# Performance work log

Measured on AMD Instinct MI355X. Metric: run time of the kernel, lower is better.

Reference implementation:

```python
import jax, jax.numpy as jnp
import numpy as np

EPS_BN = 1e-5
EPS_NORM = 1e-12


def setup_inputs() -> dict:
    dim, mid, k = 128, 32, 3
    b, h, w = 8, 128, 128
    key = jax.random.key(0)
    ks = jax.random.split(key, 16)
    s = 0.05
    return {
        "x": jax.random.normal(ks[0], (b, dim, h, w), jnp.float32),
        "w_spatial_in": jax.random.normal(ks[1], (dim, dim), jnp.float32) * s,
        "w_dw_spatial": jax.random.normal(ks[2], (dim, 1, k), jnp.float32) * s,
        "w_spatial_out": jax.random.normal(ks[3], (dim, dim), jnp.float32) * s,
        "w_ch_in": jax.random.normal(ks[4], (dim, dim), jnp.float32) * s,
        "w_ch_dw": jax.random.normal(ks[5], (dim, 1, k), jnp.float32) * s,
        "w_ch_out": jax.random.normal(ks[6], (dim, dim), jnp.float32) * s,
        "w_mlp1": jax.random.normal(ks[7], (mid, dim), jnp.float32) * s,
        "b_mlp1": jax.random.normal(ks[8], (mid,), jnp.float32) * s,
        "w_mlp2": jax.random.normal(ks[9], (dim, mid), jnp.float32) * s,
        "b_mlp2": jax.random.normal(ks[10], (dim,), jnp.float32) * s,
        "diff_weight": jnp.float32(1.0),
        "bn_gamma": jnp.ones((dim,), jnp.float32),
        "bn_beta": jnp.zeros((dim,), jnp.float32),
        "w_out_proj": jax.random.normal(ks[11], (dim, dim), jnp.float32) * s,
    }


def _dwconv1d(seq, wk):
    # seq: [b, c, L], wk: [c, 1, k] depthwise, 'same' padding
    c = seq.shape[1]
    k = wk.shape[-1]
    return jax.lax.conv_general_dilated(
        seq, wk, window_strides=(1,), padding=[(k // 2, k // 2)],
        dimension_numbers=("NCH", "OIH", "NCH"), feature_group_count=c)


def _ocs_forward(x, w_spatial_in, w_dw_spatial, w_spatial_out,
                 w_ch_in, w_ch_dw, w_ch_out,
                 w_mlp1, b_mlp1, w_mlp2, b_mlp2,
                 diff_weight, bn_gamma, bn_beta, w_out_proj):
    b, c, h, w = x.shape
    L = h * w
    alpha = beta = eta = 1.0

    # ---- scan indices (4 orders) ----
    idx_row = jnp.arange(L)
    gy, gx = jnp.meshgrid(jnp.arange(h), jnp.arange(w), indexing="ij")
    idx_col = (gx * h + gy).reshape(-1)
    orders = [idx_row, idx_row[::-1], idx_col, idx_col[::-1]]

    x_seq0 = x.reshape(b, c, L).transpose(0, 2, 1)  # [b, L, c]

    def scan(idx):
        s = x_seq0[:, idx]                                   # gather   [b,L,c]
        s = jnp.einsum("blc,oc->blo", s, w_spatial_in)       # linear
        s = _dwconv1d(s.transpose(0, 2, 1), w_dw_spatial)    # dw conv  [b,c,L]
        s = jnp.einsum("bcl,oc->blo", s, w_spatial_out)      # linear   [b,L,c]
        s = s.at[:, idx].set(s[:, jnp.arange(L)]) if False else s[:, jnp.argsort(idx)]  # scatter back (inverse perm)
        return s.transpose(0, 2, 1).reshape(b, c, h, w)

    y_sp = (scan(orders[0]) + scan(orders[1]) + scan(orders[2]) + scan(orders[3])) * 0.25

    # ---- channel branch ----
    seq = x.reshape(b, c, L)
    seq = jnp.einsum("oc,bcl->bol", w_ch_in, seq)
    seq = _dwconv1d(seq, w_ch_dw)
    seq = jnp.einsum("oc,bcl->bol", w_ch_out, seq)
    gap = x.mean((2, 3))                                     # [b,c]
    gap = gap / jnp.maximum(jnp.linalg.norm(gap, axis=1, keepdims=True), EPS_NORM)
    m = jnp.einsum("bi,bj->bij", gap, gap)                   # [b,c,c]
    seq_agg = jnp.einsum("bij,bjl->bil", m, seq)             # [b,c,L]
    h1 = jax.nn.silu(jnp.einsum("mc,bcl->bml", w_mlp1, seq_agg) + b_mlp1[None, :, None])
    y_ch = (jnp.einsum("cm,bml->bcl", w_mlp2, h1) + b_mlp2[None, :, None]).reshape(b, c, h, w)

    # ---- difference branch (reflect-pad 4-neighbor abs diff) ----
    p = jnp.pad(x, ((0, 0), (0, 0), (1, 1), (1, 1)), mode="reflect")
    cx = p[:, :, 1:-1, 1:-1]
    diff = (jnp.abs(cx - p[:, :, 1:-1, :-2]) + jnp.abs(cx - p[:, :, 1:-1, 2:])
            + jnp.abs(cx - p[:, :, :-2, 1:-1]) + jnp.abs(cx - p[:, :, 2:, 1:-1])) * 0.25
    y_diff = x + diff_weight * diff

    # ---- combine, 1x1 proj, batchnorm (training-mode batch stats) ----
    y = alpha * y_sp + beta * y_ch + eta * y_diff
    y = jnp.einsum("oc,bchw->bohw", w_out_proj, y)
    mu = y.mean((0, 2, 3))
    var = y.var((0, 2, 3))
    y = (y - mu[None, :, None, None]) * jax.lax.rsqrt(var + EPS_BN)[None, :, None, None]
    y = y * bn_gamma[None, :, None, None] + bn_beta[None, :, None, None]
    return y


def reference(x, w_spatial_in, w_dw_spatial, w_spatial_out, w_ch_in, w_ch_dw,
              w_ch_out, w_mlp1, b_mlp1, w_mlp2, b_mlp2, diff_weight,
              bn_gamma, bn_beta, w_out_proj):
    return _ocs_forward(x, w_spatial_in, w_dw_spatial, w_spatial_out,
                        w_ch_in, w_ch_dw, w_ch_out, w_mlp1, b_mlp1,
                        w_mlp2, b_mlp2, diff_weight, bn_gamma, bn_beta,
                        w_out_proj)
```

## Files before the change

kernel.cpp:

```cpp
#include <hip/hip_runtime.h>
#include <hip/hip_bf16.h>

#define C 128
#define L 16384
#define B 8
#define MID 32
#define NBL (B * L)

typedef unsigned short ushort_t;
typedef __attribute__((ext_vector_type(8))) short s8v;
typedef __attribute__((ext_vector_type(4))) float f4v;
typedef __attribute__((ext_vector_type(8))) float f8v;

__device__ __forceinline__ unsigned short f2bf(float f) {
    union { float f; unsigned int u; } a; a.f = f;
    unsigned int u = a.u;
    return (unsigned short)((u + 0x7fffu + ((u >> 16) & 1u)) >> 16);
}

__device__ __forceinline__ f8v unp8(s8v v) {
    f8v f;
#pragma unroll
    for (int j = 0; j < 8; j++) f[j] = __uint_as_float(((unsigned int)(unsigned short)v[j]) << 16);
    return f;
}

__device__ __forceinline__ f8v ldf8(const float* p) {
    float4 a = *(const float4*)p;
    float4 b = *(const float4*)(p + 4);
    f8v f;
    f[0] = a.x; f[1] = a.y; f[2] = a.z; f[3] = a.w;
    f[4] = b.x; f[5] = b.y; f[6] = b.z; f[7] = b.w;
    return f;
}

__device__ __forceinline__ int widx(int slot, int o, int w) {
    return ((slot * 8 + (o >> 4)) * 64 + (w >> 3) * 16 + (o & 15)) * 8 + (w & 7);
}

__global__ __launch_bounds__(256) void k_cvt(const float* __restrict__ x,
                                             ushort_t* __restrict__ xb,
                                             float* __restrict__ gap) {
    __shared__ float xs[64][129];
    const int bid = blockIdx.x;
    const int b = bid >> 8;
    const int l0 = (bid & 255) * 64;
    const int tid = threadIdx.x;
    const int rr = tid >> 4;
    const int col = (tid & 15) * 4;
#pragma unroll
    for (int pass = 0; pass < 8; pass++) {
        const int c = pass * 16 + rr;
        float4 v = *(const float4*)(x + ((size_t)(b * C + c)) * L + l0 + col);
        xs[col + 0][c] = v.x; xs[col + 1][c] = v.y;
        xs[col + 2][c] = v.z; xs[col + 3][c] = v.w;
    }
    __syncthreads();
    {
        const int c = tid >> 1, h = tid & 1;
        float s = 0.f;
#pragma unroll
        for (int k = 0; k < 32; k++) s += xs[h * 32 + k][c];
        s += __shfl_xor(s, 1);
        if (h == 0) atomicAdd(&gap[b * C + c], s);
    }
    const int l = tid & 63, quarter = tid >> 6, cb = quarter * 32;
    union { ushort_t hh[32]; uint4 qv[4]; } u;
#pragma unroll
    for (int k = 0; k < 32; k++) u.hh[k] = f2bf(xs[l][cb + k]);
    uint4* dst = (uint4*)(xb + ((size_t)(b * L + l0 + l)) * C + cb);
#pragma unroll
    for (int k = 0; k < 4; k++) dst[k] = u.qv[k];
}

__global__ __launch_bounds__(128) void k_prep(const float* __restrict__ Win,
                                              const float* __restrict__ Wproj,
                                              const float* __restrict__ Wout,
                                              const float* __restrict__ w2,
                                              const float* __restrict__ b2,
                                              const float* __restrict__ wds,
                                              const float* __restrict__ gap,
                                              const float* __restrict__ w1,
                                              const float* __restrict__ Wco,
                                              const float* __restrict__ wcd,
                                              const float* __restrict__ Wci,
                                              ushort_t* __restrict__ Wf,
                                              float* __restrict__ bp,
                                              float* __restrict__ a,
                                              float* __restrict__ pv) {
    const int bid = blockIdx.x;
    const int c = threadIdx.x;
    if (bid < 128) {
        const int o = bid;
        __shared__ float pr[C];
        __shared__ float wct[C];
        pr[c] = Wproj[o * C + c];
        __syncthreads();
        {
            float s = 0.f;
            for (int k = 0; k < C; k++) s = fmaf(pr[k], Wout[k * C + c], s);
            wct[c] = s;
        }
        __syncthreads();
        float a1 = 0.f, as = 0.f;
        for (int cc = 0; cc < C; cc++) {
            float w = wct[cc];
            float win = Win[cc * C + c];
            a1 = fmaf(w * wds[3 * cc + 1], win, a1);
            as = fmaf(w * (0.25f * (wds[3 * cc] + wds[3 * cc + 2])), win, as);
        }
        const int slot = c >> 5, wi = c & 31;
        Wf[widx(slot, o, wi)] = f2bf(a1);
        Wf[widx(4 + slot, o, wi)] = f2bf(as);
        Wf[widx(8 + slot, o, wi)] = f2bf(pr[c]);
        if (c < MID) {
            float s2 = 0.f;
            for (int k = 0; k < C; k++) s2 = fmaf(pr[k], w2[k * MID + c], s2);
            Wf[widx(12, o, c)] = f2bf(s2);
        }
        if (c == 0) {
            float s3 = 0.f;
            for (int k = 0; k < C; k++) s3 = fmaf(pr[k], b2[k], s3);
            bp[o] = s3;
        }
    } else {
        const int b = bid - 128;
        __shared__ float gl[C];
        __shared__ float red[C];
        __shared__ float gws[C];
        float v = gap[b * C + c] * (1.f / (float)L);
        red[c] = v * v;
        __syncthreads();
        for (int w = 64; w > 0; w >>= 1) {
            if (c < w) red[c] += red[c + w];
            __syncthreads();
        }
        float nrm = fmaxf(sqrtf(red[0]), 1e-12f);
        gl[c] = v / nrm;
        __syncthreads();
        if (c < MID) {
            float s = 0.f;
            for (int k = 0; k < C; k++) s = fmaf(w1[c * C + k], gl[k], s);
            a[b * MID + c] = s;
        }
        {
            float s = 0.f;
            for (int k = 0; k < C; k++) s = fmaf(gl[k], Wco[k * C + c], s);
            gws[c] = s;
        }
        __syncthreads();
        float p0 = 0.f, p1 = 0.f, p2 = 0.f;
        for (int cc = 0; cc < C; cc++) {
            float wv = Wci[cc * C + c];
            float g = gws[cc];
            p0 = fmaf(g * wcd[3 * cc], wv, p0);
            p1 = fmaf(g * wcd[3 * cc + 1], wv, p1);
            p2 = fmaf(g * wcd[3 * cc + 2], wv, p2);
        }
        pv[b * 384 + c] = p0;
        pv[b * 384 + 128 + c] = p1;
        pv[b * 384 + 256 + c] = p2;
    }
}

__global__ __launch_bounds__(1024) __attribute__((amdgpu_waves_per_eu(4, 4)))
void k_fused(const ushort_t* __restrict__ xb,
             const ushort_t* __restrict__ Wf,
             const float* __restrict__ pv,
             const float* __restrict__ a,
             const float* __restrict__ b1,
             const float* __restrict__ pdw,
             const float* __restrict__ bp,
             float* __restrict__ outp,
             float* __restrict__ stats) {
    __shared__ ushort_t wlf[53248];
    __shared__ float sdst[C];
    __shared__ float sdsq[C];
    const int tid = threadIdx.x;
    int bid = blockIdx.x;
    bid = (bid & 7) * 128 + (bid >> 3);
    const int b = bid >> 7;
    const int y = bid & 127;

#pragma unroll
    for (int i = 0; i < 7; i++) {
        int idx = tid + i * 1024;
        if (idx < 6656) ((uint4*)wlf)[idx] = ((const uint4*)Wf)[idx];
    }
    if (tid < C) { sdst[tid] = 0.f; sdsq[tid] = 0.f; }

    const int wave = tid >> 6, lane = tid & 63;
    const int half = wave & 1;
    const int lg = wave >> 1;
    const int n = lane & 15, q = lane >> 4;
    const int xg = lg * 16 + n;
    const int l = y * 128 + xg;
    const size_t rb = (size_t)b * L;

    const int rL = (l > 0) ? (l - 1) : -1;
    const int rR = (l < L - 1) ? (l + 1) : -1;
    const int rU = (y > 0) ? (l - 128) : ((xg > 0) ? (16256 + xg - 1) : -1);
    const int rD = (y < 127) ? (l + 128) : ((xg < 127) ? (xg + 1) : -1);
    const ushort_t* xrow = xb + (rb + l) * C;
    const ushort_t* prL = xb + (rb + ((rL >= 0) ? rL : 0)) * C;
    const ushort_t* prR = xb + (rb + ((rR >= 0) ? rR : 0)) * C;
    const ushort_t* prU = xb + (rb + ((rU >= 0) ? rU : 0)) * C;
    const ushort_t* prD = xb + (rb + ((rD >= 0) ? rD : 0)) * C;

    const float dwt4 = pdw[0] * 0.25f;

    float s1 = 0.f;
#pragma unroll
    for (int ks = 0; ks < 4; ks++) {
        const int c0 = ks * 32 + q * 8;
        {
            f8v xv = unp8(*(const s8v*)(xrow + c0));
            f8v p = ldf8(pv + b * 384 + 128 + c0);
#pragma unroll
            for (int j = 0; j < 8; j++) s1 = fmaf(p[j], xv[j], s1);
        }
        {
            f8v xv = unp8(*(const s8v*)(prL + c0));
            if (rL < 0) {
#pragma unroll
                for (int j = 0; j < 8; j++) xv[j] = 0.f;
            }
            f8v p = ldf8(pv + b * 384 + c0);
#pragma unroll
            for (int j = 0; j < 8; j++) s1 = fmaf(p[j], xv[j], s1);
        }
        {
            f8v xv = unp8(*(const s8v*)(prR + c0));
            if (rR < 0) {
#pragma unroll
                for (int j = 0; j < 8; j++) xv[j] = 0.f;
            }
            f8v p = ldf8(pv + b * 384 + 256 + c0);
#pragma unroll
            for (int j = 0; j < 8; j++) s1 = fmaf(p[j], xv[j], s1);
        }
    }
    s1 += __shfl_xor(s1, 16);
    s1 += __shfl_xor(s1, 32);

    s8v fs;
    {
        f8v av = ldf8(a + b * MID + q * 8);
        f8v bv = ldf8(b1 + q * 8);
#pragma unroll
        for (int j = 0; j < 8; j++) {
            float pre = fmaf(av[j], s1, bv[j]);
            fs[j] = (short)f2bf(pre / (1.f + __expf(-pre)));
        }
    }

    f4v acc[4];
#pragma unroll
    for (int i = 0; i < 4; i++) acc[i] = (f4v){0.f, 0.f, 0.f, 0.f};

    __syncthreads();

#define AF(slot, mtg) (*(const s8v*)(wlf + ((((slot) * 8 + (mtg)) * 64 + lane) * 8)))

#pragma unroll
    for (int mt = 0; mt < 4; mt++)
        acc[mt] = __builtin_amdgcn_mfma_f32_16x16x32_bf16(AF(12, half * 4 + mt), fs, acc[mt], 0, 0, 0);

#pragma unroll
    for (int t = 0; t < 4; t++) {
        const int r = (t == 0) ? rL : (t == 1) ? rR : (t == 2) ? rU : rD;
        const ushort_t* prow = (t == 0) ? prL : (t == 1) ? prR : (t == 2) ? prU : prD;
#pragma unroll
        for (int ks = 0; ks < 4; ks++) {
            s8v v = *(const s8v*)(prow + ks * 32 + q * 8);
            if (r < 0) v = (s8v){0, 0, 0, 0, 0, 0, 0, 0};
#pragma unroll
            for (int mt = 0; mt < 4; mt++)
                acc[mt] = __builtin_amdgcn_mfma_f32_16x16x32_bf16(AF(4 + ks, half * 4 + mt), v, acc[mt], 0, 0, 0);
        }
    }

#pragma unroll
    for (int ks = 0; ks < 4; ks++) {
        const int c0 = ks * 32 + q * 8;
        s8v vc = *(const s8v*)(xrow + c0);
#pragma unroll
        for (int mt = 0; mt < 4; mt++)
            acc[mt] = __builtin_amdgcn_mfma_f32_16x16x32_bf16(AF(ks, half * 4 + mt), vc, acc[mt], 0, 0, 0);
        f8v xc = unp8(vc);
        f8v d8;
        {
            f8v t1 = unp8(*(const s8v*)(((xg > 0) ? prL : prR) + c0));
#pragma unroll
            for (int j = 0; j < 8; j++) d8[j] = fabsf(xc[j] - t1[j]);
        }
        {
            f8v t1 = unp8(*(const s8v*)(((xg < 127) ? prR : prL) + c0));
#pragma unroll
            for (int j = 0; j < 8; j++) d8[j] += fabsf(xc[j] - t1[j]);
        }
        {
            f8v t1 = unp8(*(const s8v*)(((y > 0) ? prU : prD) + c0));
#pragma unroll
            for (int j = 0; j < 8; j++) d8[j] += fabsf(xc[j] - t1[j]);
        }
        {
            f8v t1 = unp8(*(const s8v*)(((y < 127) ? prD : prU) + c0));
#pragma unroll
            for (int j = 0; j < 8; j++) d8[j] += fabsf(xc[j] - t1[j]);
        }
        s8v vy;
#pragma unroll
        for (int j = 0; j < 8; j++) vy[j] = (short)f2bf(fmaf(dwt4, d8[j], xc[j]));
#pragma unroll
        for (int mt = 0; mt < 4; mt++)
            acc[mt] = __builtin_amdgcn_mfma_f32_16x16x32_bf16(AF(8 + ks, half * 4 + mt), vy, acc[mt], 0, 0, 0);
    }

#undef AF

#pragma unroll
    for (int mt = 0; mt < 4; mt++) {
        const int o0 = (half * 4 + mt) * 16 + q * 4;
        float4 bv4 = *(const float4*)(bp + o0);
#pragma unroll
        for (int i = 0; i < 4; i++) {
            float bai = (i == 0) ? bv4.x : (i == 1) ? bv4.y : (i == 2) ? bv4.z : bv4.w;
            float v = acc[mt][i] + bai;
            outp[((size_t)(b * C + o0 + i)) * L + l] = v;
            float s = v, sq = v * v;
            s += __shfl_xor(s, 1); sq += __shfl_xor(sq, 1);
            s += __shfl_xor(s, 2); sq += __shfl_xor(sq, 2);
            s += __shfl_xor(s, 4); sq += __shfl_xor(sq, 4);
            s += __shfl_xor(s, 8); sq += __shfl_xor(sq, 8);
            if (n == 0) {
                atomicAdd(&sdst[o0 + i], s);
                atomicAdd(&sdsq[o0 + i], sq);
            }
        }
    }
    __syncthreads();
    if (tid < C) {
        atomicAdd(&stats[tid], sdst[tid]);
        atomicAdd(&stats[C + tid], sdsq[tid]);
    }
}

__global__ __launch_bounds__(256) void k_bnapply(float* __restrict__ outp,
                                                 const float* __restrict__ stats,
                                                 const float* __restrict__ gamma,
                                                 const float* __restrict__ beta) {
    int bo = blockIdx.x;
    int o = bo & (C - 1);
    float nn = (float)NBL;
    float mu = stats[o] / nn;
    float var = stats[C + o] / nn - mu * mu;
    float sc = gamma[o] * rsqrtf(var + 1e-5f);
    float sh = fmaf(-mu, sc, beta[o]);
    float4* p = (float4*)(outp + (size_t)bo * L);
    for (int i = threadIdx.x; i < L / 4; i += 256) {
        float4 v = p[i];
        v.x = fmaf(v.x, sc, sh);
        v.y = fmaf(v.y, sc, sh);
        v.z = fmaf(v.z, sc, sh);
        v.w = fmaf(v.w, sc, sh);
        p[i] = v;
    }
}

extern "C" void kernel_launch(void* const* d_in, const int* in_sizes, int n_in,
                              void* d_out, int out_size, void* d_ws, size_t ws_size,
                              hipStream_t stream) {
    const float* x = (const float*)d_in[0];
    const float* Win = (const float*)d_in[1];
    const float* wds = (const float*)d_in[2];
    const float* Wout = (const float*)d_in[3];
    const float* Wci = (const float*)d_in[4];
    const float* wcd = (const float*)d_in[5];
    const float* Wco = (const float*)d_in[6];
    const float* w1 = (const float*)d_in[7];
    const float* b1 = (const float*)d_in[8];
    const float* w2 = (const float*)d_in[9];
    const float* b2 = (const float*)d_in[10];
    const float* pdw = (const float*)d_in[11];
    const float* gamma = (const float*)d_in[12];
    const float* beta = (const float*)d_in[13];
    const float* Wproj = (const float*)d_in[14];

    char* wsb = (char*)d_ws;
    ushort_t* xb = (ushort_t*)wsb;
    ushort_t* Wf = (ushort_t*)(wsb + 33554432);
    char* S = wsb + 176160768;
    float* gap  = (float*)(S + 0);
    float* stats= (float*)(S + 4096);
    float* a    = (float*)(S + 6144);
    float* bp   = (float*)(S + 8192);
    float* pv   = (float*)(S + 12288);
    float* outp = (float*)d_out;

    hipMemsetAsync(S, 0, 5120, stream);
    k_cvt<<<2048, 256, 0, stream>>>(x, xb, gap);
    k_prep<<<136, 128, 0, stream>>>(Win, Wproj, Wout, w2, b2, wds,
                                    gap, w1, Wco, wcd, Wci, Wf, bp, a, pv);
    k_fused<<<1024, 1024, 0, stream>>>(xb, Wf, pv, a, b1, pdw, bp, outp, stats);
    k_bnapply<<<1024, 256, 0, stream>>>(outp, stats, gamma, beta);
}
```

Measured before the change: 329.2 us.

## Split fused kernel by output half and move BN stats to separate pass

```diff
diff --git a/kernel.cpp b/kernel.cpp
--- a/kernel.cpp
+++ b/kernel.cpp
@@ -163,7 +163,7 @@
     }
 }
 
-__global__ __launch_bounds__(1024) __attribute__((amdgpu_waves_per_eu(4, 4)))
+__global__ __launch_bounds__(512) __attribute__((amdgpu_waves_per_eu(6, 6)))
 void k_fused(const ushort_t* __restrict__ xb,
              const ushort_t* __restrict__ Wf,
              const float* __restrict__ pv,
@@ -171,29 +171,27 @@
              const float* __restrict__ b1,
              const float* __restrict__ pdw,
              const float* __restrict__ bp,
-             float* __restrict__ outp,
-             float* __restrict__ stats) {
-    __shared__ ushort_t wlf[53248];
-    __shared__ float sdst[C];
-    __shared__ float sdsq[C];
+             float* __restrict__ outp) {
+    __shared__ ushort_t wlf[26624];
     const int tid = threadIdx.x;
     int bid = blockIdx.x;
-    bid = (bid & 7) * 128 + (bid >> 3);
-    const int b = bid >> 7;
-    const int y = bid & 127;
+    bid = (bid & 7) * 256 + (bid >> 3);
+    const int b = bid >> 8;
+    const int y = (bid >> 1) & 127;
+    const int half = bid & 1;
 
 #pragma unroll
     for (int i = 0; i < 7; i++) {
-        int idx = tid + i * 1024;
-        if (idx < 6656) ((uint4*)wlf)[idx] = ((const uint4*)Wf)[idx];
-    }
-    if (tid < C) { sdst[tid] = 0.f; sdsq[tid] = 0.f; }
+        int idx = tid + i * 512;
+        if (idx < 3328) {
+            int s = idx >> 8, w = idx & 255;
+            ((uint4*)wlf)[s * 256 + w] = ((const uint4*)Wf)[(s * 8 + half * 4) * 64 + w];
+        }
+    }
 
     const int wave = tid >> 6, lane = tid & 63;
-    const int half = wave & 1;
-    const int lg = wave >> 1;
     const int n = lane & 15, q = lane >> 4;
-    const int xg = lg * 16 + n;
+    const int xg = wave * 16 + n;
     const int l = y * 128 + xg;
     const size_t rb = (size_t)b * L;
 
@@ -260,11 +258,11 @@
 
     __syncthreads();
 
-#define AF(slot, mtg) (*(const s8v*)(wlf + ((((slot) * 8 + (mtg)) * 64 + lane) * 8)))
+#define AF(slot, mt) (*(const s8v*)(wlf + ((((slot) * 4 + (mt)) * 64 + lane) * 8)))
 
 #pragma unroll
     for (int mt = 0; mt < 4; mt++)
-        acc[mt] = __builtin_amdgcn_mfma_f32_16x16x32_bf16(AF(12, half * 4 + mt), fs, acc[mt], 0, 0, 0);
+        acc[mt] = __builtin_amdgcn_mfma_f32_16x16x32_bf16(AF(12, mt), fs, acc[mt], 0, 0, 0);
 
 #pragma unroll
     for (int t = 0; t < 4; t++) {
@@ -276,7 +274,7 @@
             if (r < 0) v = (s8v){0, 0, 0, 0, 0, 0, 0, 0};
 #pragma unroll
             for (int mt = 0; mt < 4; mt++)
-                acc[mt] = __builtin_amdgcn_mfma_f32_16x16x32_bf16(AF(4 + ks, half * 4 + mt), v, acc[mt], 0, 0, 0);
+                acc[mt] = __builtin_amdgcn_mfma_f32_16x16x32_bf16(AF(4 + ks, mt), v, acc[mt], 0, 0, 0);
         }
     }
 
@@ -286,7 +284,7 @@
         s8v vc = *(const s8v*)(xrow + c0);
 #pragma unroll
         for (int mt = 0; mt < 4; mt++)
-            acc[mt] = __builtin_amdgcn_mfma_f32_16x16x32_bf16(AF(ks, half * 4 + mt), vc, acc[mt], 0, 0, 0);
+            acc[mt] = __builtin_amdgcn_mfma_f32_16x16x32_bf16(AF(ks, mt), vc, acc[mt], 0, 0, 0);
         f8v xc = unp8(vc);
         f8v d8;
         {
@@ -314,7 +312,7 @@
         for (int j = 0; j < 8; j++) vy[j] = (short)f2bf(fmaf(dwt4, d8[j], xc[j]));
 #pragma unroll
         for (int mt = 0; mt < 4; mt++)
-            acc[mt] = __builtin_amdgcn_mfma_f32_16x16x32_bf16(AF(8 + ks, half * 4 + mt), vy, acc[mt], 0, 0, 0);
+            acc[mt] = __builtin_amdgcn_mfma_f32_16x16x32_bf16(AF(8 + ks, mt), vy, acc[mt], 0, 0, 0);
     }
 
 #undef AF
@@ -326,23 +324,35 @@
 #pragma unroll
         for (int i = 0; i < 4; i++) {
             float bai = (i == 0) ? bv4.x : (i == 1) ? bv4.y : (i == 2) ? bv4.z : bv4.w;
-            float v = acc[mt][i] + bai;
-            outp[((size_t)(b * C + o0 + i)) * L + l] = v;
-            float s = v, sq = v * v;
-            s += __shfl_xor(s, 1); sq += __shfl_xor(sq, 1);
-            s += __shfl_xor(s, 2); sq += __shfl_xor(sq, 2);
-            s += __shfl_xor(s, 4); sq += __shfl_xor(sq, 4);
-            s += __shfl_xor(s, 8); sq += __shfl_xor(sq, 8);
-            if (n == 0) {
-                atomicAdd(&sdst[o0 + i], s);
-                atomicAdd(&sdsq[o0 + i], sq);
-            }
-        }
-    }
+            outp[((size_t)(b * C + o0 + i)) * L + l] = acc[mt][i] + bai;
+        }
+    }
+}
+
+__global__ __launch_bounds__(256) void k_bnstats2(const float* __restrict__ outp,
+                                                  float* __restrict__ stats) {
+    const int bo = blockIdx.x;
+    const int o = bo & (C - 1);
+    const float4* p = (const float4*)(outp + (size_t)bo * L);
+    float s = 0.f, sq = 0.f;
+    for (int i = threadIdx.x; i < L / 4; i += 256) {
+        float4 v = p[i];
+        s += (v.x + v.y) + (v.z + v.w);
+        sq += v.x * v.x + v.y * v.y + v.z * v.z + v.w * v.w;
+    }
+    __shared__ float rs[256], rq[256];
+    rs[threadIdx.x] = s; rq[threadIdx.x] = sq;
     __syncthreads();
-    if (tid < C) {
-        atomicAdd(&stats[tid], sdst[tid]);
-        atomicAdd(&stats[C + tid], sdsq[tid]);
+    for (int w = 128; w > 0; w >>= 1) {
+        if (threadIdx.x < w) {
+            rs[threadIdx.x] += rs[threadIdx.x + w];
+            rq[threadIdx.x] += rq[threadIdx.x + w];
+        }
+        __syncthreads();
+    }
+    if (threadIdx.x == 0) {
+        atomicAdd(&stats[o], rs[0]);
+        atomicAdd(&stats[C + o], rq[0]);
     }
 }
 
@@ -402,6 +412,7 @@
     k_cvt<<<2048, 256, 0, stream>>>(x, xb, gap);
     k_prep<<<136, 128, 0, stream>>>(Win, Wproj, Wout, w2, b2, wds,
                                     gap, w1, Wco, wcd, Wci, Wf, bp, a, pv);
-    k_fused<<<1024, 1024, 0, stream>>>(xb, Wf, pv, a, b1, pdw, bp, outp, stats);
+    k_fused<<<2048, 512, 0, stream>>>(xb, Wf, pv, a, b1, pdw, bp, outp);
+    k_bnstats2<<<1024, 256, 0, stream>>>(outp, stats);
     k_bnapply<<<1024, 256, 0, stream>>>(outp, stats, gamma, beta);
 }
```

After: 425.7 us. 1.29x slower.
